# Kernel optimization log

Hardware: AMD Instinct MI355X
Metric: run time of the kernel (lower is better)

The kernel has to match this reference:

```python
import jax, jax.numpy as jnp
import numpy as np

N = 2_000_000
SH_C0 = 0.282095  # Y_0^0
SH_C1 = 0.488603  # Y_1^m


def setup_inputs() -> dict:
    key = jax.random.key(0)
    k1, k2, k3, k4 = jax.random.split(key, 4)
    positions = jax.random.normal(k1, (N, 3), dtype=jnp.float32)
    colors = jax.random.uniform(k2, (N, 3), dtype=jnp.float32)
    alphas = jnp.ones((N,), dtype=jnp.float32)
    R = jax.random.normal(k3, (N, 3, 3), dtype=jnp.float32)
    S = jax.random.normal(k4, (N, 3, 3), dtype=jnp.float32)
    return {"positions": positions, "colors": colors, "alphas": alphas, "R": R, "S": S}


def _sh_coeffs(colors):
    # colors: [N, 3] -> sh: [N, 4] (band-0 constant + band-1 scaled channels)
    l0 = jnp.full_like(colors[:, 0:1], SH_C0)
    l1_1 = colors[:, 1:2] * SH_C1
    l1_0 = colors[:, 0:1] * SH_C1
    l1_1n = colors[:, 2:3] * SH_C1
    return jnp.concatenate([l0, l1_1, l1_0, l1_1n], axis=1)


def reference(positions, colors, alphas, R, S):
    # Sigma = R (S S^T) R^T, per point, all [N,3,3]
    S_sq = jnp.einsum("nij,nkj->nik", S, S)          # S @ S^T
    cov = jnp.einsum("nij,njk,nlk->nil", R, S_sq, R)  # R @ S_sq @ R^T
    sh = _sh_coeffs(colors)
    return (positions, cov, alphas, sh)
```

## Files before the change

kernel.cpp:

```cpp
#include <hip/hip_runtime.h>


#define SH_C0 0.282095f
#define SH_C1 0.488603f

__global__ __launch_bounds__(256) void gs_kernel(
    const float* __restrict__ pos,
    const float* __restrict__ col,
    const float* __restrict__ alp,
    const float* __restrict__ Rm,
    const float* __restrict__ Sm,
    float* __restrict__ out_pos,
    float* __restrict__ out_cov,
    float* __restrict__ out_alp,
    float* __restrict__ out_sh,
    int n)
{
    int i = blockIdx.x * blockDim.x + threadIdx.x;
    if (i >= n) return;

    out_pos[3 * i + 0] = pos[3 * i + 0];
    out_pos[3 * i + 1] = pos[3 * i + 1];
    out_pos[3 * i + 2] = pos[3 * i + 2];

    out_alp[i] = alp[i];

    float c0 = col[3 * i + 0];
    float c1 = col[3 * i + 1];
    float c2 = col[3 * i + 2];
    out_sh[4 * i + 0] = SH_C0;
    out_sh[4 * i + 1] = c1 * SH_C1;
    out_sh[4 * i + 2] = c0 * SH_C1;
    out_sh[4 * i + 3] = c2 * SH_C1;

    float r[9], s[9];
#pragma unroll
    for (int k = 0; k < 9; ++k) r[k] = Rm[9 * i + k];
#pragma unroll
    for (int k = 0; k < 9; ++k) s[k] = Sm[9 * i + k];

    float t[9];
#pragma unroll
    for (int a = 0; a < 3; ++a) {
#pragma unroll
        for (int b = 0; b < 3; ++b) {
            t[3 * a + b] = r[3 * a + 0] * s[0 + b]
                         + r[3 * a + 1] * s[3 + b]
                         + r[3 * a + 2] * s[6 + b];
        }
    }

#pragma unroll
    for (int a = 0; a < 3; ++a) {
#pragma unroll
        for (int b = 0; b < 3; ++b) {
            out_cov[9 * i + 3 * a + b] = t[3 * a + 0] * t[3 * b + 0]
                                       + t[3 * a + 1] * t[3 * b + 1]
                                       + t[3 * a + 2] * t[3 * b + 2];
        }
    }
}

extern "C" void kernel_launch(void* const* d_in, const int* in_sizes, int n_in,
                              void* d_out, int out_size, void* d_ws, size_t ws_size,
                              hipStream_t stream) {
    const float* pos = (const float*)d_in[0];
    const float* col = (const float*)d_in[1];
    const float* alp = (const float*)d_in[2];
    const float* Rm  = (const float*)d_in[3];
    const float* Sm  = (const float*)d_in[4];

    int n = in_sizes[0] / 3;

    float* out = (float*)d_out;
    float* out_pos = out;
    float* out_cov = out + 3 * n;
    float* out_alp = out + 12 * n;
    float* out_sh  = out + 13 * n;

    int block = 256;
    int grid = (n + block - 1) / block;
    gs_kernel<<<grid, block, 0, stream>>>(pos, col, alp, Rm, Sm,
                                          out_pos, out_cov, out_alp, out_sh, n);
}
```

Measured before the change: 278.9 us.

## Process four points per thread with float4 vectorized loads and stores

Each thread now handles four consecutive points so every array is read and written as aligned float4 vectors instead of strided scalar accesses. A separate scalar tail kernel covers the leftover points when n is not a multiple of four. This is meant to cut memory instruction count and improve coalescing on a bandwidth-bound kernel. The cost is higher register use per thread (72 floats for R and S) and fewer threads overall, which may lower occupancy.

New measurement: 325.6 us. +16.8%, slower.

```diff
diff --git a/kernel.cpp b/kernel.cpp
--- a/kernel.cpp
+++ b/kernel.cpp
@@ -4,7 +4,89 @@
 #define SH_C0 0.282095f
 #define SH_C1 0.488603f
 
-__global__ __launch_bounds__(256) void gs_kernel(
+__global__ __launch_bounds__(256) void gs_kernel_v4(
+    const float4* __restrict__ pos4,
+    const float4* __restrict__ col4,
+    const float4* __restrict__ alp4,
+    const float4* __restrict__ R4,
+    const float4* __restrict__ S4,
+    float4* __restrict__ out_pos4,
+    float4* __restrict__ out_cov4,
+    float4* __restrict__ out_alp4,
+    float4* __restrict__ out_sh4,
+    int nv)
+{
+    int j = blockIdx.x * blockDim.x + threadIdx.x;
+    if (j >= nv) return;
+
+#pragma unroll
+    for (int k = 0; k < 3; ++k) out_pos4[3 * j + k] = pos4[3 * j + k];
+
+    out_alp4[j] = alp4[j];
+
+    {
+        float c[12];
+#pragma unroll
+        for (int k = 0; k < 3; ++k) {
+            float4 v = col4[3 * j + k];
+            c[4 * k + 0] = v.x; c[4 * k + 1] = v.y;
+            c[4 * k + 2] = v.z; c[4 * k + 3] = v.w;
+        }
+#pragma unroll
+        for (int p = 0; p < 4; ++p) {
+            out_sh4[4 * j + p] = make_float4(SH_C0,
+                                             c[3 * p + 1] * SH_C1,
+                                             c[3 * p + 0] * SH_C1,
+                                             c[3 * p + 2] * SH_C1);
+        }
+    }
+
+    float r[36], s[36];
+#pragma unroll
+    for (int k = 0; k < 9; ++k) {
+        float4 v = R4[9 * j + k];
+        r[4 * k + 0] = v.x; r[4 * k + 1] = v.y;
+        r[4 * k + 2] = v.z; r[4 * k + 3] = v.w;
+    }
+#pragma unroll
+    for (int k = 0; k < 9; ++k) {
+        float4 v = S4[9 * j + k];
+        s[4 * k + 0] = v.x; s[4 * k + 1] = v.y;
+        s[4 * k + 2] = v.z; s[4 * k + 3] = v.w;
+    }
+
+#pragma unroll
+    for (int p = 0; p < 4; ++p) {
+        const int o = 9 * p;
+        float t[9];
+#pragma unroll
+        for (int a = 0; a < 3; ++a) {
+#pragma unroll
+            for (int b = 0; b < 3; ++b) {
+                t[3 * a + b] = r[o + 3 * a + 0] * s[o + 0 + b]
+                             + r[o + 3 * a + 1] * s[o + 3 + b]
+                             + r[o + 3 * a + 2] * s[o + 6 + b];
+            }
+        }
+#pragma unroll
+        for (int a = 0; a < 3; ++a) {
+#pragma unroll
+            for (int b = 0; b < 3; ++b) {
+                s[o + 3 * a + b] = t[3 * a + 0] * t[3 * b + 0]
+                                 + t[3 * a + 1] * t[3 * b + 1]
+                                 + t[3 * a + 2] * t[3 * b + 2];
+            }
+        }
+    }
+
+#pragma unroll
+    for (int k = 0; k < 9; ++k) {
+        out_cov4[9 * j + k] = make_float4(s[4 * k + 0], s[4 * k + 1],
+                                          s[4 * k + 2], s[4 * k + 3]);
+    }
+}
+
+__global__ __launch_bounds__(64) void gs_kernel_tail(
     const float* __restrict__ pos,
     const float* __restrict__ col,
     const float* __restrict__ alp,
@@ -14,15 +96,14 @@
     float* __restrict__ out_cov,
     float* __restrict__ out_alp,
     float* __restrict__ out_sh,
-    int n)
+    int base, int n)
 {
-    int i = blockIdx.x * blockDim.x + threadIdx.x;
+    int i = base + threadIdx.x;
     if (i >= n) return;
 
     out_pos[3 * i + 0] = pos[3 * i + 0];
     out_pos[3 * i + 1] = pos[3 * i + 1];
     out_pos[3 * i + 2] = pos[3 * i + 2];
-
     out_alp[i] = alp[i];
 
     float c0 = col[3 * i + 0];
@@ -41,24 +122,20 @@
 
     float t[9];
 #pragma unroll
-    for (int a = 0; a < 3; ++a) {
+    for (int a = 0; a < 3; ++a)
 #pragma unroll
-        for (int b = 0; b < 3; ++b) {
+        for (int b = 0; b < 3; ++b)
             t[3 * a + b] = r[3 * a + 0] * s[0 + b]
                          + r[3 * a + 1] * s[3 + b]
                          + r[3 * a + 2] * s[6 + b];
-        }
-    }
 
 #pragma unroll
-    for (int a = 0; a < 3; ++a) {
+    for (int a = 0; a < 3; ++a)
 #pragma unroll
-        for (int b = 0; b < 3; ++b) {
+        for (int b = 0; b < 3; ++b)
             out_cov[9 * i + 3 * a + b] = t[3 * a + 0] * t[3 * b + 0]
                                        + t[3 * a + 1] * t[3 * b + 1]
                                        + t[3 * a + 2] * t[3 * b + 2];
-        }
-    }
 }
 
 extern "C" void kernel_launch(void* const* d_in, const int* in_sizes, int n_in,
@@ -78,8 +155,21 @@
     float* out_alp = out + 12 * n;
     float* out_sh  = out + 13 * n;
 
-    int block = 256;
-    int grid = (n + block - 1) / block;
-    gs_kernel<<<grid, block, 0, stream>>>(pos, col, alp, Rm, Sm,
-                                          out_pos, out_cov, out_alp, out_sh, n);
+    int nv = n / 4;
+    int rem_base = nv * 4;
+
+    if (nv > 0) {
+        int block = 256;
+        int grid = (nv + block - 1) / block;
+        gs_kernel_v4<<<grid, block, 0, stream>>>(
+            (const float4*)pos, (const float4*)col, (const float4*)alp,
+            (const float4*)Rm, (const float4*)Sm,
+            (float4*)out_pos, (float4*)out_cov, (float4*)out_alp, (float4*)out_sh,
+            nv);
+    }
+    if (rem_base < n) {
+        gs_kernel_tail<<<1, 64, 0, stream>>>(pos, col, alp, Rm, Sm,
+                                             out_pos, out_cov, out_alp, out_sh,
+                                             rem_base, n);
+    }
 }
```

## Stage per-point matrices through LDS for coalesced float4 loads and stores

Applied to the files above, without the earlier changes.

Each full block cooperatively loads its R, S, colors, positions and alphas with contiguous float4 accesses, staging R, S and colors in shared memory. It computes the covariances into shared memory, then writes them out as coalesced float4 stores. This replaces the strided per-thread 36-byte accesses, which use memory transactions poorly. A partial last block falls back to the original scalar path. The cost is about 30 KB of LDS per block and two barriers, which may lower occupancy.

New measurement: 281.7 us. About the same (+1.0%).

```diff
diff --git a/kernel.cpp b/kernel.cpp
--- a/kernel.cpp
+++ b/kernel.cpp
@@ -3,8 +3,9 @@
 
 #define SH_C0 0.282095f
 #define SH_C1 0.488603f
+#define BLK 256
 
-__global__ __launch_bounds__(256) void gs_kernel(
+__global__ __launch_bounds__(BLK) void gs_kernel(
     const float* __restrict__ pos,
     const float* __restrict__ col,
     const float* __restrict__ alp,
@@ -16,48 +17,114 @@
     float* __restrict__ out_sh,
     int n)
 {
-    int i = blockIdx.x * blockDim.x + threadIdx.x;
-    if (i >= n) return;
+    __shared__ float4 ldsR4[576];
+    __shared__ float4 ldsS4[576];
+    __shared__ float4 ldsC4[576];
+    __shared__ float4 ldsCol4[192];
 
-    out_pos[3 * i + 0] = pos[3 * i + 0];
-    out_pos[3 * i + 1] = pos[3 * i + 1];
-    out_pos[3 * i + 2] = pos[3 * i + 2];
+    const int t = threadIdx.x;
+    const int base = blockIdx.x * BLK;
 
-    out_alp[i] = alp[i];
+    if (base + BLK <= n) {
+        const float4* R4 = (const float4*)(Rm  + (size_t)base * 9);
+        const float4* S4 = (const float4*)(Sm  + (size_t)base * 9);
+        const float4* C4 = (const float4*)(col + (size_t)base * 3);
+        const float4* P4 = (const float4*)(pos + (size_t)base * 3);
+        const float4* A4 = (const float4*)(alp + (size_t)base);
+        float4* OP4 = (float4*)(out_pos + (size_t)base * 3);
+        float4* OA4 = (float4*)(out_alp + (size_t)base);
+        float4* OS4 = (float4*)(out_sh  + (size_t)base * 4);
+        float4* OC4 = (float4*)(out_cov + (size_t)base * 9);
 
-    float c0 = col[3 * i + 0];
-    float c1 = col[3 * i + 1];
-    float c2 = col[3 * i + 2];
-    out_sh[4 * i + 0] = SH_C0;
-    out_sh[4 * i + 1] = c1 * SH_C1;
-    out_sh[4 * i + 2] = c0 * SH_C1;
-    out_sh[4 * i + 3] = c2 * SH_C1;
+        ldsR4[t]       = R4[t];
+        ldsR4[t + 256] = R4[t + 256];
+        ldsS4[t]       = S4[t];
+        ldsS4[t + 256] = S4[t + 256];
+        if (t < 64) {
+            ldsR4[t + 512] = R4[t + 512];
+            ldsS4[t + 512] = S4[t + 512];
+            OA4[t] = A4[t];
+        }
+        if (t < 192) {
+            ldsCol4[t] = C4[t];
+            OP4[t] = P4[t];
+        }
 
-    float r[9], s[9];
+        __syncthreads();
+
+        const float* rf = (const float*)ldsR4 + t * 9;
+        const float* sf = (const float*)ldsS4 + t * 9;
+        float r[9], s[9];
 #pragma unroll
-    for (int k = 0; k < 9; ++k) r[k] = Rm[9 * i + k];
+        for (int k = 0; k < 9; ++k) r[k] = rf[k];
 #pragma unroll
-    for (int k = 0; k < 9; ++k) s[k] = Sm[9 * i + k];
+        for (int k = 0; k < 9; ++k) s[k] = sf[k];
 
-    float t[9];
+        float tm[9];
 #pragma unroll
-    for (int a = 0; a < 3; ++a) {
+        for (int a = 0; a < 3; ++a)
 #pragma unroll
-        for (int b = 0; b < 3; ++b) {
-            t[3 * a + b] = r[3 * a + 0] * s[0 + b]
-                         + r[3 * a + 1] * s[3 + b]
-                         + r[3 * a + 2] * s[6 + b];
-        }
-    }
+            for (int b = 0; b < 3; ++b)
+                tm[3 * a + b] = r[3 * a + 0] * s[0 + b]
+                              + r[3 * a + 1] * s[3 + b]
+                              + r[3 * a + 2] * s[6 + b];
+
+        float* cf = (float*)ldsC4 + t * 9;
+#pragma unroll
+        for (int a = 0; a < 3; ++a)
+#pragma unroll
+            for (int b = 0; b < 3; ++b)
+                cf[3 * a + b] = tm[3 * a + 0] * tm[3 * b + 0]
+                              + tm[3 * a + 1] * tm[3 * b + 1]
+                              + tm[3 * a + 2] * tm[3 * b + 2];
+
+        const float* cc = (const float*)ldsCol4 + t * 3;
+        OS4[t] = make_float4(SH_C0, cc[1] * SH_C1, cc[0] * SH_C1, cc[2] * SH_C1);
+
+        __syncthreads();
+
+        OC4[t]       = ldsC4[t];
+        OC4[t + 256] = ldsC4[t + 256];
+        if (t < 64) OC4[t + 512] = ldsC4[t + 512];
+    } else {
+        int i = base + t;
+        if (i >= n) return;
+
+        out_pos[3 * i + 0] = pos[3 * i + 0];
+        out_pos[3 * i + 1] = pos[3 * i + 1];
+        out_pos[3 * i + 2] = pos[3 * i + 2];
+        out_alp[i] = alp[i];
+
+        float c0 = col[3 * i + 0];
+        float c1 = col[3 * i + 1];
+        float c2 = col[3 * i + 2];
+        out_sh[4 * i + 0] = SH_C0;
+        out_sh[4 * i + 1] = c1 * SH_C1;
+        out_sh[4 * i + 2] = c0 * SH_C1;
+        out_sh[4 * i + 3] = c2 * SH_C1;
+
+        float r[9], s[9];
+#pragma unroll
+        for (int k = 0; k < 9; ++k) r[k] = Rm[9 * i + k];
+#pragma unroll
+        for (int k = 0; k < 9; ++k) s[k] = Sm[9 * i + k];
+
+        float tm[9];
+#pragma unroll
+        for (int a = 0; a < 3; ++a)
+#pragma unroll
+            for (int b = 0; b < 3; ++b)
+                tm[3 * a + b] = r[3 * a + 0] * s[0 + b]
+                              + r[3 * a + 1] * s[3 + b]
+                              + r[3 * a + 2] * s[6 + b];
 
 #pragma unroll
-    for (int a = 0; a < 3; ++a) {
+        for (int a = 0; a < 3; ++a)
 #pragma unroll
-        for (int b = 0; b < 3; ++b) {
-            out_cov[9 * i + 3 * a + b] = t[3 * a + 0] * t[3 * b + 0]
-                                       + t[3 * a + 1] * t[3 * b + 1]
-                                       + t[3 * a + 2] * t[3 * b + 2];
-        }
+            for (int b = 0; b < 3; ++b)
+                out_cov[9 * i + 3 * a + b] = tm[3 * a + 0] * tm[3 * b + 0]
+                                           + tm[3 * a + 1] * tm[3 * b + 1]
+                                           + tm[3 * a + 2] * tm[3 * b + 2];
     }
 }
 
@@ -78,7 +145,7 @@
     float* out_alp = out + 12 * n;
     float* out_sh  = out + 13 * n;
 
-    int block = 256;
+    int block = BLK;
     int grid = (n + block - 1) / block;
     gs_kernel<<<grid, block, 0, stream>>>(pos, col, alp, Rm, Sm,
                                           out_pos, out_cov, out_alp, out_sh, n);
```

## Split per-output work into grid-stride loops with float4 copies for pos, alpha and sh

Applied to the files above, without the earlier changes.

Restructures the kernel into separate grid-stride phases: float4 vectorized copies for positions and alphas, a float4 store for SH coefficients, and a loop for the covariance computation. The launch now uses a fixed grid of 2048 blocks. The aim is to cut per-thread scattered scalar stores and improve coalescing for the simple copy outputs. In exchange, the fixed grid reduces the number of resident threads hiding latency, and the covariance loop keeps the strided access pattern.

After: 280.4 us. About the same (+0.5%).

```diff
diff --git a/kernel.cpp b/kernel.cpp
--- a/kernel.cpp
+++ b/kernel.cpp
@@ -3,8 +3,10 @@
 
 #define SH_C0 0.282095f
 #define SH_C1 0.488603f
+#define BLK 256
+#define GRID 2048
 
-__global__ __launch_bounds__(256) void gs_kernel(
+__global__ __launch_bounds__(BLK) void gs_kernel(
     const float* __restrict__ pos,
     const float* __restrict__ col,
     const float* __restrict__ alp,
@@ -16,48 +18,59 @@
     float* __restrict__ out_sh,
     int n)
 {
-    int i = blockIdx.x * blockDim.x + threadIdx.x;
-    if (i >= n) return;
+    const int T = gridDim.x * blockDim.x;
+    const int g = blockIdx.x * blockDim.x + threadIdx.x;
 
-    out_pos[3 * i + 0] = pos[3 * i + 0];
-    out_pos[3 * i + 1] = pos[3 * i + 1];
-    out_pos[3 * i + 2] = pos[3 * i + 2];
+    {
+        const int nf = 3 * n;
+        const int n4 = nf >> 2;
+        const float4* src = (const float4*)pos;
+        float4* dst = (float4*)out_pos;
+        for (int u = g; u < n4; u += T) dst[u] = src[u];
+        for (int u = (n4 << 2) + g; u < nf; u += T) out_pos[u] = pos[u];
+    }
 
-    out_alp[i] = alp[i];
+    {
+        const int n4 = n >> 2;
+        const float4* src = (const float4*)alp;
+        float4* dst = (float4*)out_alp;
+        for (int u = g; u < n4; u += T) dst[u] = src[u];
+        for (int u = (n4 << 2) + g; u < n; u += T) out_alp[u] = alp[u];
+    }
 
-    float c0 = col[3 * i + 0];
-    float c1 = col[3 * i + 1];
-    float c2 = col[3 * i + 2];
-    out_sh[4 * i + 0] = SH_C0;
-    out_sh[4 * i + 1] = c1 * SH_C1;
-    out_sh[4 * i + 2] = c0 * SH_C1;
-    out_sh[4 * i + 3] = c2 * SH_C1;
-
-    float r[9], s[9];
-#pragma unroll
-    for (int k = 0; k < 9; ++k) r[k] = Rm[9 * i + k];
-#pragma unroll
-    for (int k = 0; k < 9; ++k) s[k] = Sm[9 * i + k];
-
-    float t[9];
-#pragma unroll
-    for (int a = 0; a < 3; ++a) {
-#pragma unroll
-        for (int b = 0; b < 3; ++b) {
-            t[3 * a + b] = r[3 * a + 0] * s[0 + b]
-                         + r[3 * a + 1] * s[3 + b]
-                         + r[3 * a + 2] * s[6 + b];
+    {
+        float4* sh4 = (float4*)out_sh;
+        for (int i = g; i < n; i += T) {
+            float c0 = col[3 * i + 0];
+            float c1 = col[3 * i + 1];
+            float c2 = col[3 * i + 2];
+            sh4[i] = make_float4(SH_C0, c1 * SH_C1, c0 * SH_C1, c2 * SH_C1);
         }
     }
 
+    for (int i = g; i < n; i += T) {
+        float r[9], s[9];
 #pragma unroll
-    for (int a = 0; a < 3; ++a) {
+        for (int k = 0; k < 9; ++k) r[k] = Rm[9 * i + k];
 #pragma unroll
-        for (int b = 0; b < 3; ++b) {
-            out_cov[9 * i + 3 * a + b] = t[3 * a + 0] * t[3 * b + 0]
-                                       + t[3 * a + 1] * t[3 * b + 1]
-                                       + t[3 * a + 2] * t[3 * b + 2];
-        }
+        for (int k = 0; k < 9; ++k) s[k] = Sm[9 * i + k];
+
+        float t[9];
+#pragma unroll
+        for (int a = 0; a < 3; ++a)
+#pragma unroll
+            for (int b = 0; b < 3; ++b)
+                t[3 * a + b] = r[3 * a + 0] * s[0 + b]
+                             + r[3 * a + 1] * s[3 + b]
+                             + r[3 * a + 2] * s[6 + b];
+
+#pragma unroll
+        for (int a = 0; a < 3; ++a)
+#pragma unroll
+            for (int b = 0; b < 3; ++b)
+                out_cov[9 * i + 3 * a + b] = t[3 * a + 0] * t[3 * b + 0]
+                                           + t[3 * a + 1] * t[3 * b + 1]
+                                           + t[3 * a + 2] * t[3 * b + 2];
     }
 }
 
@@ -78,8 +91,6 @@
     float* out_alp = out + 12 * n;
     float* out_sh  = out + 13 * n;
 
-    int block = 256;
-    int grid = (n + block - 1) / block;
-    gs_kernel<<<grid, block, 0, stream>>>(pos, col, alp, Rm, Sm,
-                                          out_pos, out_cov, out_alp, out_sh, n);
+    gs_kernel<<<GRID, BLK, 0, stream>>>(pos, col, alp, Rm, Sm,
+                                        out_pos, out_cov, out_alp, out_sh, n);
 }
```
